# Performance work log

Hardware: AMD Instinct MI355X
Metric: run time of the kernel (lower is better)

## Reference

```python
import jax, jax.numpy as jnp
import numpy as np

B, C, HS, KSEG = 64, 256, 28, 256   # batch, channels, small grid, segment-id space (mask values 0..255)
UP = 16                              # 28 -> 448 nearest upsample factor
EPS = 1e-8                           # torch.cosine_similarity eps


def setup_inputs() -> dict:
    key = jax.random.key(0)
    k1, k2, k3, k4 = jax.random.split(key, 4)
    s_feature = jax.random.normal(k1, (B, C, HS, HS), jnp.float32)
    small_s_label = (jax.random.uniform(k2, (B, 1, HS, HS)) < 0.15).astype(jnp.float32)
    q_feature = jax.random.normal(k3, (B, C, HS, HS), jnp.float32)
    small_q_mask = jax.random.randint(k4, (B, 1, HS, HS), 0, KSEG, jnp.int32)
    # full-res query mask is consistent with the 28x28 mask (original derives small from big via nearest interp)
    query_mask = jnp.repeat(jnp.repeat(small_q_mask, UP, axis=2), UP, axis=3)
    return dict(s_feature=s_feature, small_s_label=small_s_label, q_feature=q_feature,
                small_q_mask=small_q_mask, query_mask=query_mask)


def _forward(s_feature, small_s_label, q_feature, small_q_mask, query_mask):
    # support prototype; NOTE: denominator is the GLOBAL label sum (torch.sum over the whole batch), per source
    s_proto = jnp.einsum('bchw,bohw->bc', s_feature, small_s_label) / jnp.sum(small_s_label)  # [B,C]

    # vectorized segment reduce over all possible mask values (replaces per-batch/per-value Python loop)
    seg = small_q_mask[:, 0]                                   # [B,28,28] int
    onehot = jax.nn.one_hot(seg, KSEG, dtype=q_feature.dtype)  # [B,28,28,K]
    counts = onehot.sum(axis=(1, 2))                           # [B,K]
    # masked mean per segment (original scales mask by v in num and denom -> cancels to a mean)
    q_proto = jnp.einsum('bchw,bhwk->bkc', q_feature, onehot) / jnp.maximum(counts, 1.0)[..., None]  # [B,K,C]

    # cosine similarity of each query prototype with the support prototype (torch semantics, eps clamp)
    num = jnp.einsum('bc,bkc->bk', s_proto, q_proto)
    den = jnp.maximum(jnp.linalg.norm(s_proto, axis=1, keepdims=True) * jnp.linalg.norm(q_proto, axis=2), EPS)
    cos = num / den                                            # [B,K]

    v = jnp.arange(KSEG)
    present = (counts > 0) & (v[None, :] > 0)                  # nonzero segment values present in this item
    npres = present.sum(axis=1, keepdims=True)
    # keep a segment if: present AND (cos>=0 OR value==255 (skipped/always-kept) OR it is the only nonzero value)
    keep = present & ((cos >= 0) | (v[None, :] == 255) | (npres == 1))
    keepf = keep.astype(jnp.float32) * 255.0                   # [B,K]

    # scatter decision back onto the full-resolution mask via gather
    Bq, _, Hq, Wq = query_mask.shape
    idx = query_mask[:, 0].reshape(Bq, -1)                     # [B, H*W]
    final_q_mask = jnp.take_along_axis(keepf, idx, axis=1).reshape(Bq, 1, Hq, Wq)
    return final_q_mask, cos


def reference(s_feature, small_s_label, q_feature, small_q_mask, query_mask):
    return _forward(s_feature, small_s_label, q_feature, small_q_mask, query_mask)
```

## Files before the change

### kernel.cpp

```cpp
#include <hip/hip_runtime.h>

#define NB 64
#define NC 256
#define HS 28
#define NPIX 784
#define KSEG 256
#define HQ 448
#define WQ4 112
#define EPSV 1e-8f
#define CPG  4
#define NGRP 64

__global__ __launch_bounds__(256) void kMega(
    const float* __restrict__ s_feature,
    const float* __restrict__ s_label,
    const float* __restrict__ q_feature,
    const int*   __restrict__ seg,
    float* __restrict__ s_raw,
    int*   __restrict__ start_g,
    float* __restrict__ dot_part,
    float* __restrict__ qq_part)
{
    __shared__ __align__(16) float q_lds[CPG][NPIX];
    __shared__ __align__(16) int   cnt[KSEG];
    __shared__ __align__(16) int   start_lds[KSEG + 1];
    __shared__ __align__(16) unsigned short pixidx_lds[NPIX];
    __shared__ float sred4[4][CPG];

    const int t    = threadIdx.x;
    const int w    = t >> 6;
    const int lane = t & 63;
    const int g    = blockIdx.x & (NGRP - 1);
    const int b    = blockIdx.x >> 6;
    const int c0   = g * CPG;

    const float* qb = q_feature + ((size_t)(b * NC + c0)) * NPIX;
    const float* sb = s_feature + ((size_t)(b * NC + c0)) * NPIX;

    int4 sg0, sg1, sg2, sgt;
    if (w == 0) {
        const int4* sg4 = (const int4*)(seg + (size_t)b * NPIX);
        sg0 = sg4[lane];
        sg1 = sg4[lane + 64];
        sg2 = sg4[lane + 128];
        if (lane < 4) sgt = sg4[192 + lane];
    }

    float4 q0, q1, q2, q3, l4, s0, s1, s2, s3;
    if (t < 196) {
        q0 = ((const float4*)(qb + 0 * NPIX))[t];
        q1 = ((const float4*)(qb + 1 * NPIX))[t];
        q2 = ((const float4*)(qb + 2 * NPIX))[t];
        q3 = ((const float4*)(qb + 3 * NPIX))[t];
        l4 = ((const float4*)(s_label + (size_t)b * NPIX))[t];
        s0 = ((const float4*)(sb + 0 * NPIX))[t];
        s1 = ((const float4*)(sb + 1 * NPIX))[t];
        s2 = ((const float4*)(sb + 2 * NPIX))[t];
        s3 = ((const float4*)(sb + 3 * NPIX))[t];
    }
    __builtin_amdgcn_sched_barrier(0);

    if (t < 196) {
        ((float4*)&q_lds[0][0])[t] = q0;
        ((float4*)&q_lds[1][0])[t] = q1;
        ((float4*)&q_lds[2][0])[t] = q2;
        ((float4*)&q_lds[3][0])[t] = q3;
    }

    if (w == 0) {
        ((int4*)cnt)[lane] = make_int4(0, 0, 0, 0);
        atomicAdd(&cnt[sg0.x], 1); atomicAdd(&cnt[sg0.y], 1);
        atomicAdd(&cnt[sg0.z], 1); atomicAdd(&cnt[sg0.w], 1);
        atomicAdd(&cnt[sg1.x], 1); atomicAdd(&cnt[sg1.y], 1);
        atomicAdd(&cnt[sg1.z], 1); atomicAdd(&cnt[sg1.w], 1);
        atomicAdd(&cnt[sg2.x], 1); atomicAdd(&cnt[sg2.y], 1);
        atomicAdd(&cnt[sg2.z], 1); atomicAdd(&cnt[sg2.w], 1);
        if (lane < 4) {
            atomicAdd(&cnt[sgt.x], 1); atomicAdd(&cnt[sgt.y], 1);
            atomicAdd(&cnt[sgt.z], 1); atomicAdd(&cnt[sgt.w], 1);
        }
        const int4 c4 = ((const int4*)cnt)[lane];
        const int ssum = c4.x + c4.y + c4.z + c4.w;
        int incl = ssum;
        #pragma unroll
        for (int off = 1; off < 64; off <<= 1) {
            const int v = __shfl_up(incl, off, 64);
            if (lane >= off) incl += v;
        }
        const int excl = incl - ssum;
        int4 st;
        st.x = excl;
        st.y = excl + c4.x;
        st.z = st.y + c4.y;
        st.w = st.z + c4.z;
        ((int4*)start_lds)[lane] = st;
        ((int4*)cnt)[lane]       = st;
        if (lane == 63) start_lds[KSEG] = incl;
        int j_;
        j_ = atomicAdd(&cnt[sg0.x], 1); pixidx_lds[j_] = (unsigned short)(4*lane + 0);
        j_ = atomicAdd(&cnt[sg0.y], 1); pixidx_lds[j_] = (unsigned short)(4*lane + 1);
        j_ = atomicAdd(&cnt[sg0.z], 1); pixidx_lds[j_] = (unsigned short)(4*lane + 2);
        j_ = atomicAdd(&cnt[sg0.w], 1); pixidx_lds[j_] = (unsigned short)(4*lane + 3);
        j_ = atomicAdd(&cnt[sg1.x], 1); pixidx_lds[j_] = (unsigned short)(256 + 4*lane + 0);
        j_ = atomicAdd(&cnt[sg1.y], 1); pixidx_lds[j_] = (unsigned short)(256 + 4*lane + 1);
        j_ = atomicAdd(&cnt[sg1.z], 1); pixidx_lds[j_] = (unsigned short)(256 + 4*lane + 2);
        j_ = atomicAdd(&cnt[sg1.w], 1); pixidx_lds[j_] = (unsigned short)(256 + 4*lane + 3);
        j_ = atomicAdd(&cnt[sg2.x], 1); pixidx_lds[j_] = (unsigned short)(512 + 4*lane + 0);
        j_ = atomicAdd(&cnt[sg2.y], 1); pixidx_lds[j_] = (unsigned short)(512 + 4*lane + 1);
        j_ = atomicAdd(&cnt[sg2.z], 1); pixidx_lds[j_] = (unsigned short)(512 + 4*lane + 2);
        j_ = atomicAdd(&cnt[sg2.w], 1); pixidx_lds[j_] = (unsigned short)(512 + 4*lane + 3);
        if (lane < 4) {
            j_ = atomicAdd(&cnt[sgt.x], 1); pixidx_lds[j_] = (unsigned short)(768 + 4*lane + 0);
            j_ = atomicAdd(&cnt[sgt.y], 1); pixidx_lds[j_] = (unsigned short)(768 + 4*lane + 1);
            j_ = atomicAdd(&cnt[sgt.z], 1); pixidx_lds[j_] = (unsigned short)(768 + 4*lane + 2);
            j_ = atomicAdd(&cnt[sgt.w], 1); pixidx_lds[j_] = (unsigned short)(768 + 4*lane + 3);
        }
    }

    float d0 = 0.f, d1 = 0.f, d2 = 0.f, d3 = 0.f;
    if (t < 196) {
        d0 = s0.x*l4.x + s0.y*l4.y + s0.z*l4.z + s0.w*l4.w;
        d1 = s1.x*l4.x + s1.y*l4.y + s1.z*l4.z + s1.w*l4.w;
        d2 = s2.x*l4.x + s2.y*l4.y + s2.z*l4.z + s2.w*l4.w;
        d3 = s3.x*l4.x + s3.y*l4.y + s3.z*l4.z + s3.w*l4.w;
    }
    #pragma unroll
    for (int off = 32; off; off >>= 1) {
        d0 += __shfl_down(d0, off, 64);
        d1 += __shfl_down(d1, off, 64);
        d2 += __shfl_down(d2, off, 64);
        d3 += __shfl_down(d3, off, 64);
    }
    if (lane == 0) {
        sred4[w][0] = d0; sred4[w][1] = d1;
        sred4[w][2] = d2; sred4[w][3] = d3;
    }

    __syncthreads();

    if (t < CPG)
        s_raw[b * NC + c0 + t] =
            sred4[0][t] + sred4[1][t] + sred4[2][t] + sred4[3][t];
    if (g == 0) {
        start_g[b * (KSEG + 1) + t] = start_lds[t];
        if (t == 0) start_g[b * (KSEG + 1) + KSEG] = NPIX;
    }

    const int sbase = start_lds[t];
    const int send  = start_lds[t + 1];
    float a0 = 0.f, a1 = 0.f, a2 = 0.f, a3 = 0.f;
    for (int j = sbase; j < send; ++j) {
        const int p = pixidx_lds[j];
        a0 += q_lds[0][p];
        a1 += q_lds[1][p];
        a2 += q_lds[2][p];
        a3 += q_lds[3][p];
    }

    const float sc0 = sred4[0][0] + sred4[1][0] + sred4[2][0] + sred4[3][0];
    const float sc1 = sred4[0][1] + sred4[1][1] + sred4[2][1] + sred4[3][1];
    const float sc2 = sred4[0][2] + sred4[1][2] + sred4[2][2] + sred4[3][2];
    const float sc3 = sred4[0][3] + sred4[1][3] + sred4[2][3] + sred4[3][3];

    const float dot_acc = sc0*a0 + sc1*a1 + sc2*a2 + sc3*a3;
    const float qq_acc  = a0*a0 + a1*a1 + a2*a2 + a3*a3;

    const size_t o = ((size_t)b * NGRP + g) * KSEG + t;
    dot_part[o] = dot_acc;
    qq_part[o]  = qq_acc;
}

__global__ __launch_bounds__(256) void kC_cos(
    const int*   __restrict__ start_g,
    const float* __restrict__ s_raw,
    const float* __restrict__ dot_part,
    const float* __restrict__ qq_part,
    float* __restrict__ cos_out,
    float* __restrict__ keepf)
{
    __shared__ float snorm_red[4];
    __shared__ int   npres_red[4];

    const int b = blockIdx.x;
    const int k = threadIdx.x;

    const float sv = s_raw[b * NC + k];
    float s2 = sv * sv;
    for (int off = 32; off; off >>= 1) s2 += __shfl_down(s2, off, 64);
    if ((k & 63) == 0) snorm_red[k >> 6] = s2;
    __syncthreads();
    const float snorm =
        sqrtf(snorm_red[0] + snorm_red[1] + snorm_red[2] + snorm_red[3]);

    float dot = 0.0f, qq = 0.0f;
    for (int g = 0; g < NGRP; ++g) {
        const size_t o = ((size_t)b * NGRP + g) * KSEG + k;
        dot += dot_part[o];
        qq  += qq_part[o];
    }
    const float den  = fmaxf(snorm * sqrtf(qq), EPSV);
    const float cosv = dot / den;

    const int cnt_k = start_g[b * (KSEG + 1) + k + 1] - start_g[b * (KSEG + 1) + k];
    const int present = (cnt_k > 0) && (k > 0);
    int np = present;
    for (int off = 32; off; off >>= 1) np += __shfl_down(np, off, 64);
    if ((k & 63) == 0) npres_red[k >> 6] = np;
    __syncthreads();
    const int npres = npres_red[0] + npres_red[1] + npres_red[2] + npres_red[3];

    const int keep = present && ((cosv >= 0.0f) || (k == 255) || (npres == 1));
    cos_out[b * KSEG + k] = cosv;
    keepf[b * KSEG + k]   = keep ? 255.0f : 0.0f;
}

__global__ __launch_bounds__(256) void k3_gather(
    const int*   __restrict__ small_q_mask,
    const float* __restrict__ keepf,
    float4* __restrict__ out)
{
    const int gid = blockIdx.x * 256 + threadIdx.x;
    const int b   = gid / (HQ * WQ4);
    const int rem = gid % (HQ * WQ4);
    const int H   = rem / WQ4;
    const int x4  = rem % WQ4;
    const int hs  = H  >> 4;
    const int ws  = x4 >> 2;
    const int k   = small_q_mask[b * NPIX + hs * HS + ws];
    const float v = keepf[b * KSEG + k];
    out[gid] = make_float4(v, v, v, v);
}

extern "C" void kernel_launch(void* const* d_in, const int* in_sizes, int n_in,
                              void* d_out, int out_size, void* d_ws, size_t ws_size,
                              hipStream_t stream)
{
    const float* s_feature    = (const float*)d_in[0];
    const float* s_label      = (const float*)d_in[1];
    const float* q_feature    = (const float*)d_in[2];
    const int*   small_q_mask = (const int*)d_in[3];

    float* out     = (float*)d_out;
    float* cos_out = out + (size_t)NB * HQ * HQ;

    const size_t n_sraw  = (size_t)NB * NC;
    const size_t n_keepf = (size_t)NB * KSEG;
    const size_t n_start = (size_t)NB * (KSEG + 1);
    const size_t n_part  = (size_t)NB * NGRP * KSEG;

    const size_t small_elems = n_sraw + n_keepf + n_start;
    const size_t big_elems   = 2 * n_part;

    float* base = (float*)d_ws;
    float* s_raw = base;
    float* keepf = s_raw + n_sraw;
    int*   start_g = (int*)(keepf + n_keepf);

    float* bigbase;
    if (ws_size >= (small_elems + big_elems) * sizeof(float)) {
        bigbase = (float*)(start_g + n_start);
    } else {
        bigbase = out;
    }
    float* dot_part = bigbase;
    float* qq_part  = dot_part + n_part;

    kMega<<<NB * NGRP, 256, 0, stream>>>(s_feature, s_label, q_feature,
                                         small_q_mask, s_raw, start_g,
                                         dot_part, qq_part);
    kC_cos<<<NB, 256, 0, stream>>>(start_g, s_raw, dot_part, qq_part,
                                   cos_out, keepf);
    k3_gather<<<(NB * HQ * WQ4) / 256, 256, 0, stream>>>(small_q_mask, keepf,
                                                         (float4*)d_out);
}
```

Measured before the change: 40.82 us.

## Hoist per-batch segment sort into separate kernel and double channels per block

```diff
diff --git a/kernel.cpp b/kernel.cpp
--- a/kernel.cpp
+++ b/kernel.cpp
@@ -8,55 +8,98 @@
 #define HQ 448
 #define WQ4 112
 #define EPSV 1e-8f
-#define CPG  4
-#define NGRP 64
+#define CPG  8
+#define NGRP 32
+
+__global__ __launch_bounds__(256) void kA_sort(
+    const int* __restrict__ seg,
+    int* __restrict__ start_g,
+    unsigned short* __restrict__ pixidx_g)
+{
+    __shared__ int cnt[KSEG];
+    __shared__ int scan[KSEG];
+    __shared__ int cursor[KSEG];
+
+    const int b = blockIdx.x;
+    const int t = threadIdx.x;
+    const int* sg = seg + (size_t)b * NPIX;
+
+    cnt[t] = 0;
+    __syncthreads();
+    for (int p = t; p < NPIX; p += 256) atomicAdd(&cnt[sg[p]], 1);
+    __syncthreads();
+
+    scan[t] = cnt[t];
+    __syncthreads();
+    for (int d = 1; d < KSEG; d <<= 1) {
+        int v = (t >= d) ? scan[t - d] : 0;
+        __syncthreads();
+        scan[t] += v;
+        __syncthreads();
+    }
+    const int startv = scan[t] - cnt[t];
+    start_g[b * (KSEG + 1) + t] = startv;
+    if (t == 0) start_g[b * (KSEG + 1) + KSEG] = NPIX;
+
+    cursor[t] = startv;
+    __syncthreads();
+    for (int p = t; p < NPIX; p += 256) {
+        const int j = atomicAdd(&cursor[sg[p]], 1);
+        pixidx_g[b * NPIX + j] = (unsigned short)p;
+    }
+}
 
 __global__ __launch_bounds__(256) void kMega(
     const float* __restrict__ s_feature,
     const float* __restrict__ s_label,
     const float* __restrict__ q_feature,
-    const int*   __restrict__ seg,
+    const int*   __restrict__ start_g,
+    const unsigned short* __restrict__ pixidx_g,
     float* __restrict__ s_raw,
-    int*   __restrict__ start_g,
     float* __restrict__ dot_part,
     float* __restrict__ qq_part)
 {
     __shared__ __align__(16) float q_lds[CPG][NPIX];
-    __shared__ __align__(16) int   cnt[KSEG];
+    __shared__ __align__(16) unsigned short pixidx_lds[NPIX];
     __shared__ __align__(16) int   start_lds[KSEG + 1];
-    __shared__ __align__(16) unsigned short pixidx_lds[NPIX];
     __shared__ float sred4[4][CPG];
 
     const int t    = threadIdx.x;
     const int w    = t >> 6;
     const int lane = t & 63;
     const int g    = blockIdx.x & (NGRP - 1);
-    const int b    = blockIdx.x >> 6;
+    const int b    = blockIdx.x >> 5;
     const int c0   = g * CPG;
 
     const float* qb = q_feature + ((size_t)(b * NC + c0)) * NPIX;
     const float* sb = s_feature + ((size_t)(b * NC + c0)) * NPIX;
 
-    int4 sg0, sg1, sg2, sgt;
-    if (w == 0) {
-        const int4* sg4 = (const int4*)(seg + (size_t)b * NPIX);
-        sg0 = sg4[lane];
-        sg1 = sg4[lane + 64];
-        sg2 = sg4[lane + 128];
-        if (lane < 4) sgt = sg4[192 + lane];
-    }
-
-    float4 q0, q1, q2, q3, l4, s0, s1, s2, s3;
+    float4 q0, q1, q2, q3, q4, q5, q6, q7;
+    int4   px;
+    float4 l4, s0, s1, s2, s3, s4, s5, s6, s7;
     if (t < 196) {
         q0 = ((const float4*)(qb + 0 * NPIX))[t];
         q1 = ((const float4*)(qb + 1 * NPIX))[t];
         q2 = ((const float4*)(qb + 2 * NPIX))[t];
         q3 = ((const float4*)(qb + 3 * NPIX))[t];
+        q4 = ((const float4*)(qb + 4 * NPIX))[t];
+        q5 = ((const float4*)(qb + 5 * NPIX))[t];
+        q6 = ((const float4*)(qb + 6 * NPIX))[t];
+        q7 = ((const float4*)(qb + 7 * NPIX))[t];
+    }
+    if (t < 98)
+        px = ((const int4*)(pixidx_g + (size_t)b * NPIX))[t];
+    const int stv = start_g[b * (KSEG + 1) + t];
+    if (t < 196) {
         l4 = ((const float4*)(s_label + (size_t)b * NPIX))[t];
         s0 = ((const float4*)(sb + 0 * NPIX))[t];
         s1 = ((const float4*)(sb + 1 * NPIX))[t];
         s2 = ((const float4*)(sb + 2 * NPIX))[t];
         s3 = ((const float4*)(sb + 3 * NPIX))[t];
+        s4 = ((const float4*)(sb + 4 * NPIX))[t];
+        s5 = ((const float4*)(sb + 5 * NPIX))[t];
+        s6 = ((const float4*)(sb + 6 * NPIX))[t];
+        s7 = ((const float4*)(sb + 7 * NPIX))[t];
     }
     __builtin_amdgcn_sched_barrier(0);
 
@@ -65,64 +108,26 @@
         ((float4*)&q_lds[1][0])[t] = q1;
         ((float4*)&q_lds[2][0])[t] = q2;
         ((float4*)&q_lds[3][0])[t] = q3;
-    }
-
-    if (w == 0) {
-        ((int4*)cnt)[lane] = make_int4(0, 0, 0, 0);
-        atomicAdd(&cnt[sg0.x], 1); atomicAdd(&cnt[sg0.y], 1);
-        atomicAdd(&cnt[sg0.z], 1); atomicAdd(&cnt[sg0.w], 1);
-        atomicAdd(&cnt[sg1.x], 1); atomicAdd(&cnt[sg1.y], 1);
-        atomicAdd(&cnt[sg1.z], 1); atomicAdd(&cnt[sg1.w], 1);
-        atomicAdd(&cnt[sg2.x], 1); atomicAdd(&cnt[sg2.y], 1);
-        atomicAdd(&cnt[sg2.z], 1); atomicAdd(&cnt[sg2.w], 1);
-        if (lane < 4) {
-            atomicAdd(&cnt[sgt.x], 1); atomicAdd(&cnt[sgt.y], 1);
-            atomicAdd(&cnt[sgt.z], 1); atomicAdd(&cnt[sgt.w], 1);
-        }
-        const int4 c4 = ((const int4*)cnt)[lane];
-        const int ssum = c4.x + c4.y + c4.z + c4.w;
-        int incl = ssum;
-        #pragma unroll
-        for (int off = 1; off < 64; off <<= 1) {
-            const int v = __shfl_up(incl, off, 64);
-            if (lane >= off) incl += v;
-        }
-        const int excl = incl - ssum;
-        int4 st;
-        st.x = excl;
-        st.y = excl + c4.x;
-        st.z = st.y + c4.y;
-        st.w = st.z + c4.z;
-        ((int4*)start_lds)[lane] = st;
-        ((int4*)cnt)[lane]       = st;
-        if (lane == 63) start_lds[KSEG] = incl;
-        int j_;
-        j_ = atomicAdd(&cnt[sg0.x], 1); pixidx_lds[j_] = (unsigned short)(4*lane + 0);
-        j_ = atomicAdd(&cnt[sg0.y], 1); pixidx_lds[j_] = (unsigned short)(4*lane + 1);
-        j_ = atomicAdd(&cnt[sg0.z], 1); pixidx_lds[j_] = (unsigned short)(4*lane + 2);
-        j_ = atomicAdd(&cnt[sg0.w], 1); pixidx_lds[j_] = (unsigned short)(4*lane + 3);
-        j_ = atomicAdd(&cnt[sg1.x], 1); pixidx_lds[j_] = (unsigned short)(256 + 4*lane + 0);
-        j_ = atomicAdd(&cnt[sg1.y], 1); pixidx_lds[j_] = (unsigned short)(256 + 4*lane + 1);
-        j_ = atomicAdd(&cnt[sg1.z], 1); pixidx_lds[j_] = (unsigned short)(256 + 4*lane + 2);
-        j_ = atomicAdd(&cnt[sg1.w], 1); pixidx_lds[j_] = (unsigned short)(256 + 4*lane + 3);
-        j_ = atomicAdd(&cnt[sg2.x], 1); pixidx_lds[j_] = (unsigned short)(512 + 4*lane + 0);
-        j_ = atomicAdd(&cnt[sg2.y], 1); pixidx_lds[j_] = (unsigned short)(512 + 4*lane + 1);
-        j_ = atomicAdd(&cnt[sg2.z], 1); pixidx_lds[j_] = (unsigned short)(512 + 4*lane + 2);
-        j_ = atomicAdd(&cnt[sg2.w], 1); pixidx_lds[j_] = (unsigned short)(512 + 4*lane + 3);
-        if (lane < 4) {
-            j_ = atomicAdd(&cnt[sgt.x], 1); pixidx_lds[j_] = (unsigned short)(768 + 4*lane + 0);
-            j_ = atomicAdd(&cnt[sgt.y], 1); pixidx_lds[j_] = (unsigned short)(768 + 4*lane + 1);
-            j_ = atomicAdd(&cnt[sgt.z], 1); pixidx_lds[j_] = (unsigned short)(768 + 4*lane + 2);
-            j_ = atomicAdd(&cnt[sgt.w], 1); pixidx_lds[j_] = (unsigned short)(768 + 4*lane + 3);
-        }
-    }
+        ((float4*)&q_lds[4][0])[t] = q4;
+        ((float4*)&q_lds[5][0])[t] = q5;
+        ((float4*)&q_lds[6][0])[t] = q6;
+        ((float4*)&q_lds[7][0])[t] = q7;
+    }
+    if (t < 98) ((int4*)pixidx_lds)[t] = px;
+    start_lds[t] = stv;
+    if (t == 0) start_lds[KSEG] = NPIX;
 
     float d0 = 0.f, d1 = 0.f, d2 = 0.f, d3 = 0.f;
+    float d4 = 0.f, d5 = 0.f, d6 = 0.f, d7 = 0.f;
     if (t < 196) {
         d0 = s0.x*l4.x + s0.y*l4.y + s0.z*l4.z + s0.w*l4.w;
         d1 = s1.x*l4.x + s1.y*l4.y + s1.z*l4.z + s1.w*l4.w;
         d2 = s2.x*l4.x + s2.y*l4.y + s2.z*l4.z + s2.w*l4.w;
         d3 = s3.x*l4.x + s3.y*l4.y + s3.z*l4.z + s3.w*l4.w;
+        d4 = s4.x*l4.x + s4.y*l4.y + s4.z*l4.z + s4.w*l4.w;
+        d5 = s5.x*l4.x + s5.y*l4.y + s5.z*l4.z + s5.w*l4.w;
+        d6 = s6.x*l4.x + s6.y*l4.y + s6.z*l4.z + s6.w*l4.w;
+        d7 = s7.x*l4.x + s7.y*l4.y + s7.z*l4.z + s7.w*l4.w;
     }
     #pragma unroll
     for (int off = 32; off; off >>= 1) {
@@ -130,10 +135,14 @@
         d1 += __shfl_down(d1, off, 64);
         d2 += __shfl_down(d2, off, 64);
         d3 += __shfl_down(d3, off, 64);
+        d4 += __shfl_down(d4, off, 64);
+        d5 += __shfl_down(d5, off, 64);
+        d6 += __shfl_down(d6, off, 64);
+        d7 += __shfl_down(d7, off, 64);
     }
     if (lane == 0) {
-        sred4[w][0] = d0; sred4[w][1] = d1;
-        sred4[w][2] = d2; sred4[w][3] = d3;
+        sred4[w][0] = d0; sred4[w][1] = d1; sred4[w][2] = d2; sred4[w][3] = d3;
+        sred4[w][4] = d4; sred4[w][5] = d5; sred4[w][6] = d6; sred4[w][7] = d7;
     }
 
     __syncthreads();
@@ -141,29 +150,36 @@
     if (t < CPG)
         s_raw[b * NC + c0 + t] =
             sred4[0][t] + sred4[1][t] + sred4[2][t] + sred4[3][t];
-    if (g == 0) {
-        start_g[b * (KSEG + 1) + t] = start_lds[t];
-        if (t == 0) start_g[b * (KSEG + 1) + KSEG] = NPIX;
-    }
 
     const int sbase = start_lds[t];
     const int send  = start_lds[t + 1];
     float a0 = 0.f, a1 = 0.f, a2 = 0.f, a3 = 0.f;
+    float a4 = 0.f, a5 = 0.f, a6 = 0.f, a7 = 0.f;
     for (int j = sbase; j < send; ++j) {
         const int p = pixidx_lds[j];
         a0 += q_lds[0][p];
         a1 += q_lds[1][p];
         a2 += q_lds[2][p];
         a3 += q_lds[3][p];
+        a4 += q_lds[4][p];
+        a5 += q_lds[5][p];
+        a6 += q_lds[6][p];
+        a7 += q_lds[7][p];
     }
 
     const float sc0 = sred4[0][0] + sred4[1][0] + sred4[2][0] + sred4[3][0];
     const float sc1 = sred4[0][1] + sred4[1][1] + sred4[2][1] + sred4[3][1];
     const float sc2 = sred4[0][2] + sred4[1][2] + sred4[2][2] + sred4[3][2];
     const float sc3 = sred4[0][3] + sred4[1][3] + sred4[2][3] + sred4[3][3];
-
-    const float dot_acc = sc0*a0 + sc1*a1 + sc2*a2 + sc3*a3;
-    const float qq_acc  = a0*a0 + a1*a1 + a2*a2 + a3*a3;
+    const float sc4 = sred4[0][4] + sred4[1][4] + sred4[2][4] + sred4[3][4];
+    const float sc5 = sred4[0][5] + sred4[1][5] + sred4[2][5] + sred4[3][5];
+    const float sc6 = sred4[0][6] + sred4[1][6] + sred4[2][6] + sred4[3][6];
+    const float sc7 = sred4[0][7] + sred4[1][7] + sred4[2][7] + sred4[3][7];
+
+    const float dot_acc = sc0*a0 + sc1*a1 + sc2*a2 + sc3*a3
+                        + sc4*a4 + sc5*a5 + sc6*a6 + sc7*a7;
+    const float qq_acc  = a0*a0 + a1*a1 + a2*a2 + a3*a3
+                        + a4*a4 + a5*a5 + a6*a6 + a7*a7;
 
     const size_t o = ((size_t)b * NGRP + g) * KSEG + t;
     dot_part[o] = dot_acc;
@@ -246,28 +262,31 @@
     const size_t n_sraw  = (size_t)NB * NC;
     const size_t n_keepf = (size_t)NB * KSEG;
     const size_t n_start = (size_t)NB * (KSEG + 1);
+    const size_t n_pix32 = (size_t)NB * NPIX / 2;
     const size_t n_part  = (size_t)NB * NGRP * KSEG;
 
-    const size_t small_elems = n_sraw + n_keepf + n_start;
+    const size_t small_elems = n_sraw + n_keepf + n_start + n_pix32;
     const size_t big_elems   = 2 * n_part;
 
     float* base = (float*)d_ws;
     float* s_raw = base;
     float* keepf = s_raw + n_sraw;
     int*   start_g = (int*)(keepf + n_keepf);
+    unsigned short* pixidx_g = (unsigned short*)(start_g + n_start);
 
     float* bigbase;
     if (ws_size >= (small_elems + big_elems) * sizeof(float)) {
-        bigbase = (float*)(start_g + n_start);
+        bigbase = (float*)d_ws + small_elems;
     } else {
         bigbase = out;
     }
     float* dot_part = bigbase;
     float* qq_part  = dot_part + n_part;
 
+    kA_sort<<<NB, 256, 0, stream>>>(small_q_mask, start_g, pixidx_g);
     kMega<<<NB * NGRP, 256, 0, stream>>>(s_feature, s_label, q_feature,
-                                         small_q_mask, s_raw, start_g,
-                                         dot_part, qq_part);
+                                         start_g, pixidx_g,
+                                         s_raw, dot_part, qq_part);
     kC_cos<<<NB, 256, 0, stream>>>(start_g, s_raw, dot_part, qq_part,
                                    cos_out, keepf);
     k3_gather<<<(NB * HQ * WQ4) / 256, 256, 0, stream>>>(small_q_mask, keepf,
```

New measurement: 41.86 us. 2.5% more time.
